# Kernel optimization log

Measured on AMD Instinct MI355X. Metric: run time of the kernel, lower is better.

Reference implementation:

```python
import jax, jax.numpy as jnp
import numpy as np

B, S, D = 2, 2048, 1024
H = 16
HD = D // H  # head_dim = 64
NEG = -1e30  # finite stand-in for -inf; masked entries are zeroed after softmax so math matches


def setup_inputs() -> dict:
    key = jax.random.key(0)
    ks = jax.random.split(key, 10)
    q = jax.random.normal(ks[0], (B, S, D), dtype=jnp.float32)
    k = jax.random.normal(ks[1], (B, S, D), dtype=jnp.float32)
    v = jax.random.normal(ks[2], (B, S, D), dtype=jnp.float32)
    mask = jax.random.randint(ks[3], (B, S), 0, 2).astype(bool)
    s = 1.0 / np.sqrt(D)
    Wq = jax.random.uniform(ks[4], (D, D), jnp.float32, -s, s)
    bq = jax.random.uniform(ks[5], (D,), jnp.float32, -s, s)
    Wk = jax.random.uniform(ks[6], (D, D), jnp.float32, -s, s)
    bk = jax.random.uniform(ks[7], (D,), jnp.float32, -s, s)
    Wv = jax.random.uniform(ks[8], (D, D), jnp.float32, -s, s)
    bv = jax.random.uniform(ks[9], (D,), jnp.float32, -s, s)
    return {"q": q, "k": k, "v": v, "mask": mask,
            "Wq": Wq, "bq": bq, "Wk": Wk, "bk": bk, "Wv": Wv, "bv": bv}


def _split_heads(x):
    # [B,S,D] -> [H,B,S,HD]  (matches permute(2,0,1,3) in torch)
    return x.reshape(B, S, H, HD).transpose(2, 0, 1, 3)


def reference(q, k, v, mask, Wq, bq, Wk, bk, Wv, bv):
    mq = _split_heads(q @ Wq.T + bq)
    mk = _split_heads(k @ Wk.T + bk)
    mv = _split_heads(v @ Wv.T + bv)
    # scores: [H,B,Sq,Sk]
    scores = jnp.einsum('hbqd,hbkd->hbqk', mq, mk) / jnp.sqrt(jnp.float32(HD))
    pair_mask = (mask[:, :, None] & mask[:, None, :])[None]  # [1,B,S,S]
    scores = jnp.where(pair_mask, scores, NEG)
    attn = jax.nn.softmax(scores, axis=-1)
    attn = jnp.where(pair_mask, attn, 0.0)
    out = jnp.einsum('hbqk,hbkd->hbqd', attn, mv)
    # [H,B,S,HD] -> [B,S,D]
    return out.transpose(1, 2, 0, 3).reshape(B, S, H * HD)
```

## Files before the change

### kernel.cpp

```cpp
#include <hip/hip_runtime.h>
#include <math.h>

#define B_ 2
#define S_ 2048
#define D_ 1024
#define H_ 16
#define HD_ 64
#define LOG2E 1.44269504088896340736f

typedef __bf16 bf16_t;
typedef bf16_t bf16x8 __attribute__((ext_vector_type(8)));
typedef bf16_t bf16x4v __attribute__((ext_vector_type(4)));
typedef float f32x4 __attribute__((ext_vector_type(4)));

#define GLOBAL_LOAD_LDS16(gp, lp)                                              \
    __builtin_amdgcn_global_load_lds(                                          \
        (const __attribute__((address_space(1))) void*)(gp),                   \
        (__attribute__((address_space(3))) void*)(lp), 16, 0, 0)

__global__ __launch_bounds__(256) void cvt_kernel(
    const float* __restrict__ q, const float* __restrict__ k,
    const float* __restrict__ v, const float* __restrict__ wq,
    const float* __restrict__ wk, const float* __restrict__ wv,
    const int* __restrict__ msk,
    bf16_t* __restrict__ qb, bf16_t* __restrict__ kb, bf16_t* __restrict__ vb,
    bf16_t* __restrict__ wqb, bf16_t* __restrict__ wkb, bf16_t* __restrict__ wvb,
    float* __restrict__ kbias)
{
    const size_t NT = (size_t)1 << 20;
    const size_t NW = (size_t)1 << 18;
    size_t g = (size_t)blockIdx.x * 256 + threadIdx.x;

    const float* src;
    bf16_t* dst;
    size_t off;
    if (g < 3 * NT) {
        int t = (int)(g >> 20);
        off = (g & (NT - 1)) * 4;
        src = (t == 0) ? q : (t == 1) ? k : v;
        dst = (t == 0) ? qb : (t == 1) ? kb : vb;
    } else if (g < 3 * NT + 3 * NW) {
        size_t gw = g - 3 * NT;
        int t = (int)(gw >> 18);
        off = (gw & (NW - 1)) * 4;
        src = (t == 0) ? wq : (t == 1) ? wk : wv;
        dst = (t == 0) ? wqb : (t == 1) ? wkb : wvb;
    } else {
        size_t gm = g - (3 * NT + 3 * NW);
        if (gm >= (size_t)B_ * S_ / 4) return;
        size_t idx = gm * 4;
        int4 mi = *(const int4*)(msk + idx);
        float4 o4;
        const float VB = -8.0f * LOG2E;
        const float MB = -1.44269504e30f;
        o4.x = mi.x ? VB : MB;
        o4.y = mi.y ? VB : MB;
        o4.z = mi.z ? VB : MB;
        o4.w = mi.w ? VB : MB;
        *(float4*)(kbias + idx) = o4;
        return;
    }

    float4 f = *(const float4*)(src + off);
    bf16x4v o;
    o[0] = (bf16_t)f.x; o[1] = (bf16_t)f.y;
    o[2] = (bf16_t)f.z; o[3] = (bf16_t)f.w;
    *(bf16x4v*)(dst + off) = o;
}

__global__ __launch_bounds__(256) void proj_mfma(
    const bf16_t* __restrict__ X0, const bf16_t* __restrict__ X1,
    const bf16_t* __restrict__ X2, const bf16_t* __restrict__ W0,
    const bf16_t* __restrict__ W1, const bf16_t* __restrict__ W2,
    const float* __restrict__ b0, const float* __restrict__ b1,
    const float* __restrict__ b2, bf16_t* __restrict__ o0,
    bf16_t* __restrict__ o1, bf16_t* __restrict__ o2)
{
    __shared__ __align__(16) bf16_t As[2][128 * 32];
    __shared__ __align__(16) bf16_t Bs[2][128 * 32];

    const int orig = blockIdx.x + 32 * blockIdx.y + 256 * blockIdx.z;
    const int work = (orig & 7) * 96 + (orig >> 3);
    const int bx = work & 31;
    const int by = (work >> 5) & 7;
    const int z  = work >> 8;

    const bf16_t* X = (z == 0) ? X0 : (z == 1) ? X1 : X2;
    const bf16_t* W = (z == 0) ? W0 : (z == 1) ? W1 : W2;
    const float* bias = (z == 0) ? b0 : (z == 1) ? b1 : b2;
    bf16_t* out = (z == 0) ? o0 : (z == 1) ? o1 : o2;
    const float oscale = (z == 0) ? (0.125f * LOG2E) : 1.0f;

    const int tid  = threadIdx.x;
    const int w    = tid >> 6;
    const int lane = tid & 63;
    const int L    = lane & 15;
    const int quad = lane >> 4;
    const int wr   = (w >> 1) * 64;
    const int wc   = (w & 1) * 64;
    const int row0 = bx * 128;
    const int col0 = by * 128;

    const int lr = lane >> 2;
    const int lc = (lane & 3) * 8;

    f32x4 acc[4][4];
    #pragma unroll
    for (int i = 0; i < 4; ++i)
        #pragma unroll
        for (int j = 0; j < 4; ++j) {
            acc[i][j][0] = 0.f; acc[i][j][1] = 0.f;
            acc[i][j][2] = 0.f; acc[i][j][3] = 0.f;
        }

    #pragma unroll
    for (int i = 0; i < 2; ++i) {
        const int rA = i * 64 + w * 16;
        GLOBAL_LOAD_LDS16(X + (size_t)(row0 + rA + lr) * D_ + lc, &As[0][rA * 32]);
        GLOBAL_LOAD_LDS16(W + (size_t)(col0 + rA + lr) * D_ + lc, &Bs[0][rA * 32]);
    }
    __syncthreads();

    for (int kk = 0; kk < 32; ++kk) {
        const int cur = kk & 1;
        if (kk < 31) {
            const int k0 = (kk + 1) * 32;
            #pragma unroll
            for (int i = 0; i < 2; ++i) {
                const int rA = i * 64 + w * 16;
                GLOBAL_LOAD_LDS16(X + (size_t)(row0 + rA + lr) * D_ + k0 + lc,
                                  &As[cur ^ 1][rA * 32]);
                GLOBAL_LOAD_LDS16(W + (size_t)(col0 + rA + lr) * D_ + k0 + lc,
                                  &Bs[cur ^ 1][rA * 32]);
            }
        }

        bf16x8 aF[4], bF[4];
        #pragma unroll
        for (int t = 0; t < 4; ++t) {
            aF[t] = *(const bf16x8*)&As[cur][(wr + t * 16 + L) * 32 + quad * 8];
            bF[t] = *(const bf16x8*)&Bs[cur][(wc + t * 16 + L) * 32 + quad * 8];
        }
        #pragma unroll
        for (int mt = 0; mt < 4; ++mt)
            #pragma unroll
            for (int nt = 0; nt < 4; ++nt)
                acc[mt][nt] = __builtin_amdgcn_mfma_f32_16x16x32_bf16(
                    aF[mt], bF[nt], acc[mt][nt], 0, 0, 0);

        __syncthreads();
    }

    if (z == 2) {
        #pragma unroll
        for (int nt = 0; nt < 4; ++nt) {
            const int j  = col0 + wc + nt * 16 + L;
            const float bval = bias[j];
            const int h  = j >> 6;
            const int hd = j & 63;
            #pragma unroll
            for (int mt = 0; mt < 4; ++mt) {
                const int n0 = row0 + wr + mt * 16 + quad * 4;
                const int b  = n0 >> 11;
                const int s  = n0 & (S_ - 1);
                bf16x4v p;
                #pragma unroll
                for (int r = 0; r < 4; ++r)
                    p[r] = (bf16_t)(acc[mt][nt][r] + bval);
                *(bf16x4v*)(out + ((size_t)(b * H_ + h) * HD_ + hd) * S_ + s) = p;
            }
        }
    } else {
        #pragma unroll
        for (int nt = 0; nt < 4; ++nt) {
            const int j  = col0 + wc + nt * 16 + L;
            const float bval = bias[j];
            const int h  = j >> 6;
            const int hd = j & 63;
            #pragma unroll
            for (int mt = 0; mt < 4; ++mt)
                #pragma unroll
                for (int r = 0; r < 4; ++r) {
                    const int n = row0 + wr + mt * 16 + quad * 4 + r;
                    const int b = n >> 11;
                    const int s = n & (S_ - 1);
                    out[((((size_t)b * H_ + h) * S_ + s) * HD_) + hd] =
                        (bf16_t)((acc[mt][nt][r] + bval) * oscale);
                }
        }
    }
}

__global__ __launch_bounds__(256) void attn_kernel(
    const bf16_t* __restrict__ Q, const bf16_t* __restrict__ K,
    const bf16_t* __restrict__ Vt, const float* __restrict__ kbias,
    const int* __restrict__ mask, float* __restrict__ out)
{
    __shared__ bf16_t Ks[2][64 * 64];
    __shared__ bf16_t Vs[2][64 * 64];
    __shared__ bf16_t Pt[4][32 * 64];

    const int tid  = threadIdx.x;
    const int w    = tid >> 6;
    const int lane = tid & 63;
    const int L    = lane & 15;
    const int quad = lane >> 4;
    const int L7   = L & 7;

    const int orig = blockIdx.x + 16 * (blockIdx.y + 16 * blockIdx.z);
    const int work = (orig & 7) * 64 + (orig >> 3);
    const int q0   = (work & 15) * 128;
    const int h    = (work >> 4) & 15;
    const int b    = work >> 8;
    const int bh   = b * H_ + h;

    const bf16_t* kbase = K  + (size_t)bh * S_ * HD_;
    const bf16_t* vbase = Vt + (size_t)bh * HD_ * S_;
    const float*  bbase = kbias + b * S_;
    const int*    mrow  = mask + b * S_;

    const int sr  = tid >> 3;
    const int c8  = tid & 7;
    const int sc2 = c8 * 8;
    const int swz = ((c8 ^ (sr & 7)) * 8);
    const int st0 = sr * 64 + swz;
    const int st1 = (sr + 32) * 64 + swz;

    bf16x8 aQ[2][2];
    #pragma unroll
    for (int qb = 0; qb < 2; ++qb) {
        const bf16_t* qp = Q + ((size_t)bh * S_ + q0 + w * 32 + qb * 16 + L) * HD_;
        aQ[qb][0] = *(const bf16x8*)(qp + quad * 8);
        aQ[qb][1] = *(const bf16x8*)(qp + 32 + quad * 8);
    }

    f32x4 o[2][4];
    #pragma unroll
    for (int qb = 0; qb < 2; ++qb)
        #pragma unroll
        for (int f = 0; f < 4; ++f) {
            o[qb][f][0]=0.f; o[qb][f][1]=0.f; o[qb][f][2]=0.f; o[qb][f][3]=0.f;
        }
    f32x4 ol[2];
    #pragma unroll
    for (int qb = 0; qb < 2; ++qb) {
        ol[qb][0]=0.f; ol[qb][1]=0.f; ol[qb][2]=0.f; ol[qb][3]=0.f;
    }

    bf16x8 ones;
    #pragma unroll
    for (int i = 0; i < 8; ++i) ones[i] = (bf16_t)1.0f;

    bf16x8 kr0, kr1, vr0, vr1;
    f32x4  bias_c[4], bias_n[4];
    kr0 = *(const bf16x8*)(kbase + (size_t)sr * HD_ + sc2);
    kr1 = *(const bf16x8*)(kbase + (size_t)(sr + 32) * HD_ + sc2);
    vr0 = *(const bf16x8*)(vbase + (size_t)sr * S_ + sc2);
    vr1 = *(const bf16x8*)(vbase + (size_t)(sr + 32) * S_ + sc2);
    #pragma unroll
    for (int f = 0; f < 4; ++f)
        bias_c[f] = *(const f32x4*)(bbase + f * 16 + quad * 4);

    *(bf16x8*)&Ks[0][st0] = kr0;
    *(bf16x8*)&Ks[0][st1] = kr1;
    *(bf16x8*)&Vs[0][st0] = vr0;
    *(bf16x8*)&Vs[0][st1] = vr1;

    kr0 = *(const bf16x8*)(kbase + (size_t)(64 + sr) * HD_ + sc2);
    kr1 = *(const bf16x8*)(kbase + (size_t)(64 + sr + 32) * HD_ + sc2);
    vr0 = *(const bf16x8*)(vbase + (size_t)sr * S_ + 64 + sc2);
    vr1 = *(const bf16x8*)(vbase + (size_t)(sr + 32) * S_ + 64 + sc2);
    #pragma unroll
    for (int f = 0; f < 4; ++f)
        bias_n[f] = *(const f32x4*)(bbase + 64 + f * 16 + quad * 4);

    __syncthreads();

    for (int t = 0; t < 32; ++t) {
        const int cur = t & 1;
        bf16_t* ks  = &Ks[cur][0];
        bf16_t* vs  = &Vs[cur][0];

        if (t < 31) {
            bf16_t* ksn = &Ks[cur ^ 1][0];
            bf16_t* vsn = &Vs[cur ^ 1][0];
            *(bf16x8*)&ksn[st0] = kr0;
            *(bf16x8*)&ksn[st1] = kr1;
            *(bf16x8*)&vsn[st0] = vr0;
            *(bf16x8*)&vsn[st1] = vr1;
        }
        if (t < 30) {
            const int kn = (t + 2) * 64;
            kr0 = *(const bf16x8*)(kbase + (size_t)(kn + sr) * HD_ + sc2);
            kr1 = *(const bf16x8*)(kbase + (size_t)(kn + sr + 32) * HD_ + sc2);
            vr0 = *(const bf16x8*)(vbase + (size_t)sr * S_ + kn + sc2);
            vr1 = *(const bf16x8*)(vbase + (size_t)(sr + 32) * S_ + kn + sc2);
        }

        bf16x8 aK[4][2];
        #pragma unroll
        for (int f = 0; f < 4; ++f) {
            const int row = (f * 16 + L) * 64;
            aK[f][0] = *(const bf16x8*)&ks[row + ((quad ^ L7) * 8)];
            aK[f][1] = *(const bf16x8*)&ks[row + (((4 | quad) ^ L7) * 8)];
        }

        bf16_t* pw = &Pt[w][0];
        #pragma unroll
        for (int qb = 0; qb < 2; ++qb) {
            const int prow = (qb * 16 + L) * 64;
            #pragma unroll
            for (int f = 0; f < 4; ++f) {
                f32x4 z = bias_c[f];
                z = __builtin_amdgcn_mfma_f32_16x16x32_bf16(aK[f][0], aQ[qb][0], z, 0, 0, 0);
                z = __builtin_amdgcn_mfma_f32_16x16x32_bf16(aK[f][1], aQ[qb][1], z, 0, 0, 0);
                bf16x4v p4;
                p4[0] = (bf16_t)exp2f(z[0]);
                p4[1] = (bf16_t)exp2f(z[1]);
                p4[2] = (bf16_t)exp2f(z[2]);
                p4[3] = (bf16_t)exp2f(z[3]);
                *(bf16x4v*)&pw[prow + (((f * 2 + (quad >> 1)) ^ L7) * 8) + (quad & 1) * 4] = p4;
            }
        }

        #pragma unroll
        for (int f = 0; f < 4; ++f) bias_c[f] = bias_n[f];
        if (t < 30) {
            const int kn = (t + 2) * 64;
            #pragma unroll
            for (int f = 0; f < 4; ++f)
                bias_n[f] = *(const f32x4*)(bbase + kn + f * 16 + quad * 4);
        }

        bf16x8 aP[2][2];
        #pragma unroll
        for (int qb = 0; qb < 2; ++qb) {
            const int prow = (qb * 16 + L) * 64;
            aP[qb][0] = *(const bf16x8*)&pw[prow + ((quad ^ L7) * 8)];
            aP[qb][1] = *(const bf16x8*)&pw[prow + (((4 | quad) ^ L7) * 8)];
            ol[qb] = __builtin_amdgcn_mfma_f32_16x16x32_bf16(aP[qb][0], ones, ol[qb], 0, 0, 0);
            ol[qb] = __builtin_amdgcn_mfma_f32_16x16x32_bf16(aP[qb][1], ones, ol[qb], 0, 0, 0);
        }

        #pragma unroll
        for (int f = 0; f < 4; ++f) {
            const int row = (f * 16 + L) * 64;
            bf16x8 bV0 = *(const bf16x8*)&vs[row + ((quad ^ L7) * 8)];
            bf16x8 bV1 = *(const bf16x8*)&vs[row + (((4 | quad) ^ L7) * 8)];
            #pragma unroll
            for (int qb = 0; qb < 2; ++qb) {
                o[qb][f] = __builtin_amdgcn_mfma_f32_16x16x32_bf16(aP[qb][0], bV0, o[qb][f], 0, 0, 0);
                o[qb][f] = __builtin_amdgcn_mfma_f32_16x16x32_bf16(aP[qb][1], bV1, o[qb][f], 0, 0, 0);
            }
        }

        __syncthreads();
    }

    #pragma unroll
    for (int qb = 0; qb < 2; ++qb) {
        const int4 m4 = *(const int4*)&mrow[q0 + w * 32 + qb * 16 + quad * 4];
        float inv[4];
        inv[0] = (m4.x && ol[qb][0] > 0.f) ? (1.0f / ol[qb][0]) : 0.0f;
        inv[1] = (m4.y && ol[qb][1] > 0.f) ? (1.0f / ol[qb][1]) : 0.0f;
        inv[2] = (m4.z && ol[qb][2] > 0.f) ? (1.0f / ol[qb][2]) : 0.0f;
        inv[3] = (m4.w && ol[qb][3] > 0.f) ? (1.0f / ol[qb][3]) : 0.0f;

        float* obase = out + ((size_t)b * S_ + q0 + w * 32 + qb * 16 + quad * 4) * D_ + h * HD_;
        #pragma unroll
        for (int f = 0; f < 4; ++f)
            #pragma unroll
            for (int r = 0; r < 4; ++r)
                obase[r * D_ + f * 16 + L] = o[qb][f][r] * inv[r];
    }
}

extern "C" void kernel_launch(void* const* d_in, const int* in_sizes, int n_in,
                              void* d_out, int out_size, void* d_ws, size_t ws_size,
                              hipStream_t stream)
{
    const float* q    = (const float*)d_in[0];
    const float* k    = (const float*)d_in[1];
    const float* v    = (const float*)d_in[2];
    const int*   mask = (const int*)d_in[3];
    const float* Wq   = (const float*)d_in[4];
    const float* bq   = (const float*)d_in[5];
    const float* Wk   = (const float*)d_in[6];
    const float* bk   = (const float*)d_in[7];
    const float* Wv   = (const float*)d_in[8];
    const float* bv   = (const float*)d_in[9];
    float* out = (float*)d_out;

    const size_t PE = (size_t)B_ * S_ * D_;
    const size_t WE = (size_t)D_ * D_;

    bf16_t* qb    = (bf16_t*)d_ws;
    bf16_t* kb    = qb + PE;
    bf16_t* vb    = kb + PE;
    bf16_t* wqb   = vb + PE;
    bf16_t* wkb   = wqb + WE;
    bf16_t* wvb   = wkb + WE;
    bf16_t* mq    = wvb + WE;
    bf16_t* mk    = mq + PE;
    bf16_t* vt    = mk + PE;
    float*  kbias = (float*)(vt + PE);

    const size_t ngroups = 3 * (PE / 4) + 3 * (WE / 4) + (size_t)B_ * S_ / 4;
    dim3 cgrid((ngroups + 255) / 256);
    cvt_kernel<<<cgrid, 256, 0, stream>>>(q, k, v, Wq, Wk, Wv, mask,
                                          qb, kb, vb, wqb, wkb, wvb, kbias);

    dim3 pgrid(4096 / 128, 1024 / 128, 3);
    proj_mfma<<<pgrid, 256, 0, stream>>>(qb, kb, vb, wqb, wkb, wvb,
                                         bq, bk, bv, mq, mk, vt);

    dim3 agrid(S_ / 128, H_, B_);
    attn_kernel<<<agrid, 256, 0, stream>>>(mq, mk, vt, kbias, mask, out);
}
```

Measured before the change: 232.9 us.

## Fuse fp32-to-bf16 activation conversion into projection GEMM and inline mask bias

The projection kernel now reads fp32 activations directly, converting them to bf16 in registers before storing to LDS, with a register prefetch two k-steps ahead. The separate conversion pass over q/k/v and its bf16 workspace round-trip are removed, so that kernel only converts the weights. The attention kernel now builds the key bias from the int mask on the fly instead of reading a precomputed bias array, and uses raw v_exp_f32 in place of exp2f. The projection grid also drops its block-swizzle remap. In exchange, the A-operand loads are synchronous register loads instead of async global-to-LDS loads, and the loss of the swizzle may change cache reuse.

After: 239.2 us. +2.7%, slower.

```diff
diff --git a/kernel.cpp b/kernel.cpp
--- a/kernel.cpp
+++ b/kernel.cpp
@@ -18,48 +18,26 @@
         (const __attribute__((address_space(1))) void*)(gp),                   \
         (__attribute__((address_space(3))) void*)(lp), 16, 0, 0)
 
+static __device__ __forceinline__ float exp2_raw(float x)
+{
+    float r;
+    asm("v_exp_f32 %0, %1" : "=v"(r) : "v"(x));
+    return r;
+}
+
 __global__ __launch_bounds__(256) void cvt_kernel(
-    const float* __restrict__ q, const float* __restrict__ k,
-    const float* __restrict__ v, const float* __restrict__ wq,
-    const float* __restrict__ wk, const float* __restrict__ wv,
-    const int* __restrict__ msk,
-    bf16_t* __restrict__ qb, bf16_t* __restrict__ kb, bf16_t* __restrict__ vb,
-    bf16_t* __restrict__ wqb, bf16_t* __restrict__ wkb, bf16_t* __restrict__ wvb,
-    float* __restrict__ kbias)
+    const float* __restrict__ wq, const float* __restrict__ wk,
+    const float* __restrict__ wv,
+    bf16_t* __restrict__ wqb, bf16_t* __restrict__ wkb, bf16_t* __restrict__ wvb)
 {
-    const size_t NT = (size_t)1 << 20;
     const size_t NW = (size_t)1 << 18;
     size_t g = (size_t)blockIdx.x * 256 + threadIdx.x;
-
-    const float* src;
-    bf16_t* dst;
-    size_t off;
-    if (g < 3 * NT) {
-        int t = (int)(g >> 20);
-        off = (g & (NT - 1)) * 4;
-        src = (t == 0) ? q : (t == 1) ? k : v;
-        dst = (t == 0) ? qb : (t == 1) ? kb : vb;
-    } else if (g < 3 * NT + 3 * NW) {
-        size_t gw = g - 3 * NT;
-        int t = (int)(gw >> 18);
-        off = (gw & (NW - 1)) * 4;
-        src = (t == 0) ? wq : (t == 1) ? wk : wv;
-        dst = (t == 0) ? wqb : (t == 1) ? wkb : wvb;
-    } else {
-        size_t gm = g - (3 * NT + 3 * NW);
-        if (gm >= (size_t)B_ * S_ / 4) return;
-        size_t idx = gm * 4;
-        int4 mi = *(const int4*)(msk + idx);
-        float4 o4;
-        const float VB = -8.0f * LOG2E;
-        const float MB = -1.44269504e30f;
-        o4.x = mi.x ? VB : MB;
-        o4.y = mi.y ? VB : MB;
-        o4.z = mi.z ? VB : MB;
-        o4.w = mi.w ? VB : MB;
-        *(float4*)(kbias + idx) = o4;
-        return;
-    }
+    if (g >= 3 * NW) return;
+
+    int t = (int)(g >> 18);
+    size_t off = (g & (NW - 1)) * 4;
+    const float* src = (t == 0) ? wq : (t == 1) ? wk : wv;
+    bf16_t* dst      = (t == 0) ? wqb : (t == 1) ? wkb : wvb;
 
     float4 f = *(const float4*)(src + off);
     bf16x4v o;
@@ -69,8 +47,8 @@
 }
 
 __global__ __launch_bounds__(256) void proj_mfma(
-    const bf16_t* __restrict__ X0, const bf16_t* __restrict__ X1,
-    const bf16_t* __restrict__ X2, const bf16_t* __restrict__ W0,
+    const float* __restrict__ X0, const float* __restrict__ X1,
+    const float* __restrict__ X2, const bf16_t* __restrict__ W0,
     const bf16_t* __restrict__ W1, const bf16_t* __restrict__ W2,
     const float* __restrict__ b0, const float* __restrict__ b1,
     const float* __restrict__ b2, bf16_t* __restrict__ o0,
@@ -79,13 +57,8 @@
     __shared__ __align__(16) bf16_t As[2][128 * 32];
     __shared__ __align__(16) bf16_t Bs[2][128 * 32];
 
-    const int orig = blockIdx.x + 32 * blockIdx.y + 256 * blockIdx.z;
-    const int work = (orig & 7) * 96 + (orig >> 3);
-    const int bx = work & 31;
-    const int by = (work >> 5) & 7;
-    const int z  = work >> 8;
-
-    const bf16_t* X = (z == 0) ? X0 : (z == 1) ? X1 : X2;
+    const int z = blockIdx.z;
+    const float*  X = (z == 0) ? X0 : (z == 1) ? X1 : X2;
     const bf16_t* W = (z == 0) ? W0 : (z == 1) ? W1 : W2;
     const float* bias = (z == 0) ? b0 : (z == 1) ? b1 : b2;
     bf16_t* out = (z == 0) ? o0 : (z == 1) ? o1 : o2;
@@ -98,11 +71,13 @@
     const int quad = lane >> 4;
     const int wr   = (w >> 1) * 64;
     const int wc   = (w & 1) * 64;
-    const int row0 = bx * 128;
-    const int col0 = by * 128;
+    const int row0 = blockIdx.x * 128;
+    const int col0 = blockIdx.y * 128;
 
     const int lr = lane >> 2;
     const int lc = (lane & 3) * 8;
+    const int arow = tid >> 3;
+    const int ac4  = (tid & 7) * 4;
 
     f32x4 acc[4][4];
     #pragma unroll
@@ -113,26 +88,53 @@
             acc[i][j][2] = 0.f; acc[i][j][3] = 0.f;
         }
 
+    float4 ax[4];
+    const float* xbase = X + (size_t)(row0 + arow) * D_ + ac4;
+
+    #pragma unroll
+    for (int rr = 0; rr < 4; ++rr)
+        ax[rr] = *(const float4*)(xbase + (size_t)rr * 32 * D_);
+    #pragma unroll
+    for (int rr = 0; rr < 4; ++rr) {
+        bf16x4v t4;
+        t4[0] = (bf16_t)ax[rr].x; t4[1] = (bf16_t)ax[rr].y;
+        t4[2] = (bf16_t)ax[rr].z; t4[3] = (bf16_t)ax[rr].w;
+        *(bf16x4v*)&As[0][(arow + rr * 32) * 32 + ac4] = t4;
+    }
     #pragma unroll
     for (int i = 0; i < 2; ++i) {
         const int rA = i * 64 + w * 16;
-        GLOBAL_LOAD_LDS16(X + (size_t)(row0 + rA + lr) * D_ + lc, &As[0][rA * 32]);
         GLOBAL_LOAD_LDS16(W + (size_t)(col0 + rA + lr) * D_ + lc, &Bs[0][rA * 32]);
     }
+    #pragma unroll
+    for (int rr = 0; rr < 4; ++rr)
+        ax[rr] = *(const float4*)(xbase + (size_t)rr * 32 * D_ + 32);
     __syncthreads();
 
     for (int kk = 0; kk < 32; ++kk) {
         const int cur = kk & 1;
+
         if (kk < 31) {
-            const int k0 = (kk + 1) * 32;
+            #pragma unroll
+            for (int rr = 0; rr < 4; ++rr) {
+                bf16x4v t4;
+                t4[0] = (bf16_t)ax[rr].x; t4[1] = (bf16_t)ax[rr].y;
+                t4[2] = (bf16_t)ax[rr].z; t4[3] = (bf16_t)ax[rr].w;
+                *(bf16x4v*)&As[cur ^ 1][(arow + rr * 32) * 32 + ac4] = t4;
+            }
+            const int k1 = (kk + 1) * 32;
             #pragma unroll
             for (int i = 0; i < 2; ++i) {
                 const int rA = i * 64 + w * 16;
-                GLOBAL_LOAD_LDS16(X + (size_t)(row0 + rA + lr) * D_ + k0 + lc,
-                                  &As[cur ^ 1][rA * 32]);
-                GLOBAL_LOAD_LDS16(W + (size_t)(col0 + rA + lr) * D_ + k0 + lc,
+                GLOBAL_LOAD_LDS16(W + (size_t)(col0 + rA + lr) * D_ + k1 + lc,
                                   &Bs[cur ^ 1][rA * 32]);
             }
+        }
+        if (kk < 30) {
+            const int k2 = (kk + 2) * 32;
+            #pragma unroll
+            for (int rr = 0; rr < 4; ++rr)
+                ax[rr] = *(const float4*)(xbase + (size_t)rr * 32 * D_ + k2);
         }
 
         bf16x8 aF[4], bF[4];
@@ -193,8 +195,8 @@
 
 __global__ __launch_bounds__(256) void attn_kernel(
     const bf16_t* __restrict__ Q, const bf16_t* __restrict__ K,
-    const bf16_t* __restrict__ Vt, const float* __restrict__ kbias,
-    const int* __restrict__ mask, float* __restrict__ out)
+    const bf16_t* __restrict__ Vt, const int* __restrict__ mask,
+    float* __restrict__ out)
 {
     __shared__ bf16_t Ks[2][64 * 64];
     __shared__ bf16_t Vs[2][64 * 64];
@@ -207,6 +209,9 @@
     const int quad = lane >> 4;
     const int L7   = L & 7;
 
+    const float VB = -8.0f * LOG2E;
+    const float MB = -1.44269504e30f;
+
     const int orig = blockIdx.x + 16 * (blockIdx.y + 16 * blockIdx.z);
     const int work = (orig & 7) * 64 + (orig >> 3);
     const int q0   = (work & 15) * 128;
@@ -216,7 +221,6 @@
 
     const bf16_t* kbase = K  + (size_t)bh * S_ * HD_;
     const bf16_t* vbase = Vt + (size_t)bh * HD_ * S_;
-    const float*  bbase = kbias + b * S_;
     const int*    mrow  = mask + b * S_;
 
     const int sr  = tid >> 3;
@@ -258,8 +262,13 @@
     vr0 = *(const bf16x8*)(vbase + (size_t)sr * S_ + sc2);
     vr1 = *(const bf16x8*)(vbase + (size_t)(sr + 32) * S_ + sc2);
     #pragma unroll
-    for (int f = 0; f < 4; ++f)
-        bias_c[f] = *(const f32x4*)(bbase + f * 16 + quad * 4);
+    for (int f = 0; f < 4; ++f) {
+        int4 mi = *(const int4*)(mrow + f * 16 + quad * 4);
+        bias_c[f][0] = mi.x ? VB : MB;
+        bias_c[f][1] = mi.y ? VB : MB;
+        bias_c[f][2] = mi.z ? VB : MB;
+        bias_c[f][3] = mi.w ? VB : MB;
+    }
 
     *(bf16x8*)&Ks[0][st0] = kr0;
     *(bf16x8*)&Ks[0][st1] = kr1;
@@ -271,8 +280,13 @@
     vr0 = *(const bf16x8*)(vbase + (size_t)sr * S_ + 64 + sc2);
     vr1 = *(const bf16x8*)(vbase + (size_t)(sr + 32) * S_ + 64 + sc2);
     #pragma unroll
-    for (int f = 0; f < 4; ++f)
-        bias_n[f] = *(const f32x4*)(bbase + 64 + f * 16 + quad * 4);
+    for (int f = 0; f < 4; ++f) {
+        int4 mi = *(const int4*)(mrow + 64 + f * 16 + quad * 4);
+        bias_n[f][0] = mi.x ? VB : MB;
+        bias_n[f][1] = mi.y ? VB : MB;
+        bias_n[f][2] = mi.z ? VB : MB;
+        bias_n[f][3] = mi.w ? VB : MB;
+    }
 
     __syncthreads();
 
@@ -315,10 +329,10 @@
                 z = __builtin_amdgcn_mfma_f32_16x16x32_bf16(aK[f][0], aQ[qb][0], z, 0, 0, 0);
                 z = __builtin_amdgcn_mfma_f32_16x16x32_bf16(aK[f][1], aQ[qb][1], z, 0, 0, 0);
                 bf16x4v p4;
-                p4[0] = (bf16_t)exp2f(z[0]);
-                p4[1] = (bf16_t)exp2f(z[1]);
-                p4[2] = (bf16_t)exp2f(z[2]);
-                p4[3] = (bf16_t)exp2f(z[3]);
+                p4[0] = (bf16_t)exp2_raw(z[0]);
+                p4[1] = (bf16_t)exp2_raw(z[1]);
+                p4[2] = (bf16_t)exp2_raw(z[2]);
+                p4[3] = (bf16_t)exp2_raw(z[3]);
                 *(bf16x4v*)&pw[prow + (((f * 2 + (quad >> 1)) ^ L7) * 8) + (quad & 1) * 4] = p4;
             }
         }
@@ -328,8 +342,13 @@
         if (t < 30) {
             const int kn = (t + 2) * 64;
             #pragma unroll
-            for (int f = 0; f < 4; ++f)
-                bias_n[f] = *(const f32x4*)(bbase + kn + f * 16 + quad * 4);
+            for (int f = 0; f < 4; ++f) {
+                int4 mi = *(const int4*)(mrow + kn + f * 16 + quad * 4);
+                bias_n[f][0] = mi.x ? VB : MB;
+                bias_n[f][1] = mi.y ? VB : MB;
+                bias_n[f][2] = mi.z ? VB : MB;
+                bias_n[f][3] = mi.w ? VB : MB;
+            }
         }
 
         bf16x8 aP[2][2];
@@ -394,26 +413,20 @@
     const size_t PE = (size_t)B_ * S_ * D_;
     const size_t WE = (size_t)D_ * D_;
 
-    bf16_t* qb    = (bf16_t*)d_ws;
-    bf16_t* kb    = qb + PE;
-    bf16_t* vb    = kb + PE;
-    bf16_t* wqb   = vb + PE;
-    bf16_t* wkb   = wqb + WE;
-    bf16_t* wvb   = wkb + WE;
-    bf16_t* mq    = wvb + WE;
-    bf16_t* mk    = mq + PE;
-    bf16_t* vt    = mk + PE;
-    float*  kbias = (float*)(vt + PE);
-
-    const size_t ngroups = 3 * (PE / 4) + 3 * (WE / 4) + (size_t)B_ * S_ / 4;
-    dim3 cgrid((ngroups + 255) / 256);
-    cvt_kernel<<<cgrid, 256, 0, stream>>>(q, k, v, Wq, Wk, Wv, mask,
-                                          qb, kb, vb, wqb, wkb, wvb, kbias);
+    bf16_t* wqb = (bf16_t*)d_ws;
+    bf16_t* wkb = wqb + WE;
+    bf16_t* wvb = wkb + WE;
+    bf16_t* mq  = wvb + WE;
+    bf16_t* mk  = mq + PE;
+    bf16_t* vt  = mk + PE;
+
+    dim3 cgrid(3 * (WE / 4) / 256);
+    cvt_kernel<<<cgrid, 256, 0, stream>>>(Wq, Wk, Wv, wqb, wkb, wvb);
 
     dim3 pgrid(4096 / 128, 1024 / 128, 3);
-    proj_mfma<<<pgrid, 256, 0, stream>>>(qb, kb, vb, wqb, wkb, wvb,
+    proj_mfma<<<pgrid, 256, 0, stream>>>(q, k, v, wqb, wkb, wvb,
                                          bq, bk, bv, mq, mk, vt);
 
     dim3 agrid(S_ / 128, H_, B_);
-    attn_kernel<<<agrid, 256, 0, stream>>>(mq, mk, vt, kbias, mask, out);
+    attn_kernel<<<agrid, 256, 0, stream>>>(mq, mk, vt, mask, out);
 }
```
